# Kernel tuning notes

Measured on AMD Instinct MI355X. Metric: run time of the kernel, lower is better.

The kernel has to match this reference:

```python
import jax, jax.numpy as jnp
import numpy as np

U = 512  # units

def hard_sigmoid(x):
    # Keras hard_sigmoid: clip(0.2*x + 0.5, 0, 1)
    return jnp.clip(0.2 * x + 0.5, 0.0, 1.0)

def setup_inputs() -> dict:
    key = jax.random.key(0)
    ks = jax.random.split(key, 9)
    B, T, A, D = 64, 2048, 512, 512  # batch, annotation steps, annotation units, input dim
    s = lambda k, shape, scale: jax.random.normal(k, shape, jnp.float32) * scale
    return {
        "inputs": s(ks[0], (B, D), 1.0),
        "h": s(ks[1], (B, U), 1.0),
        "c": s(ks[2], (B, U), 1.0),
        "annotations": s(ks[3], (B, T, A), 1.0),
        "kernel": s(ks[4], (D + A, 4 * U), 0.02),
        "recurrent_kernel": s(ks[5], (U, 4 * U), 0.02),
        "bias": jnp.zeros((6 * U,), jnp.float32).at[U:2 * U].set(1.0),  # unit_forget_bias
        "kernel_u": s(ks[6], (A, U), 0.02),
        "kernel_w": s(ks[7], (U, U), 0.02),
        "kernel_v": s(ks[8], (U,), 0.02),
    }

def reference(inputs, h, c, annotations, kernel, recurrent_kernel, bias, kernel_u, kernel_w, kernel_v):
    bias_u = bias[4 * U:5 * U]
    # precomputed annotation projection (done once in build()): [B,T,U]
    uh = jnp.einsum('bta,au->btu', annotations, kernel_u) + bias_u
    # Bahdanau attention scores
    Wxstm = h @ kernel_w                                   # [B,U]
    et = jnp.einsum('btu,u->bt', jnp.tanh(uh + Wxstm[:, None, :]), kernel_v)
    at = jax.nn.softmax(et, axis=1)                        # exp/sum in source == softmax
    context = jnp.einsum('bt,bta->ba', at, annotations)    # [B,A]
    x = jnp.concatenate([inputs, context], axis=-1)        # [B, D+A]
    z = x @ kernel + h @ recurrent_kernel + bias[:4 * U]   # [B,4U]
    i = hard_sigmoid(z[:, :U])
    f = hard_sigmoid(z[:, U:2 * U])
    c_new = f * c + i * jnp.tanh(z[:, 2 * U:3 * U])
    o = hard_sigmoid(z[:, 3 * U:])
    h_new = o * jnp.tanh(c_new)
    return h_new
```

## Files before the change

### kernel.cpp

```cpp
#include <hip/hip_runtime.h>

constexpr int U = 512;
constexpr int B = 64;
constexpr int T = 2048;
constexpr int A = 512;

typedef __attribute__((ext_vector_type(8))) short short8;
typedef __attribute__((ext_vector_type(4))) float f32x4;

__device__ __forceinline__ unsigned short f32_to_bf16(float f) {
    unsigned int b = __float_as_uint(f);
    unsigned int r = (b + 0x7FFFu + ((b >> 16) & 1u)) >> 16;
    return (unsigned short)r;
}

__device__ __forceinline__ float fast_tanh(float x) {
    float e = exp2f(x * 2.885390081777927f);
    return (e - 1.0f) * __builtin_amdgcn_rcpf(e + 1.0f);
}

__device__ __forceinline__ float hard_sigmoid(float z) {
    return fminf(fmaxf(0.2f * z + 0.5f, 0.0f), 1.0f);
}

__global__ __launch_bounds__(256) void k_prep_s(const float* __restrict__ h,
                                                const float* __restrict__ kw,
                                                float* __restrict__ Sp) {
    int b = blockIdx.x >> 2;
    int kc = blockIdx.x & 3;
    int u = threadIdx.x;
    const float* hb = h + b * U + kc * 128;
    const float* kwb = kw + (size_t)kc * 128 * U;
    float a0 = 0.f, a1 = 0.f;
#pragma unroll 4
    for (int k = 0; k < 128; ++k) {
        float hv = hb[k];
        a0 += hv * kwb[(size_t)k * U + u];
        a1 += hv * kwb[(size_t)k * U + u + 256];
    }
    float* p = Sp + ((size_t)kc * 64 + b) * U;
    p[u] = a0;
    p[u + 256] = a1;
}

__global__ __launch_bounds__(256) void k_s_reduce(const float* __restrict__ Sp,
                                                  const float* __restrict__ bias,
                                                  float* __restrict__ S) {
    int gid = blockIdx.x * 256 + threadIdx.x;
    int b = gid >> 9, u = gid & 511;
    float s = bias[4 * U + u];
#pragma unroll
    for (int kc = 0; kc < 4; ++kc) s += Sp[((size_t)kc * 64 + b) * U + u];
    S[gid] = s;
}

__global__ __launch_bounds__(256) void k_prep_kut(const float* __restrict__ ku,
                                                  unsigned short* __restrict__ kut) {
    __shared__ float tile[32][33];
    int a0 = (blockIdx.x >> 4) << 5;
    int u0 = (blockIdx.x & 15) << 5;
    int c = threadIdx.x & 31, r0 = threadIdx.x >> 5;
#pragma unroll
    for (int p = 0; p < 4; ++p) {
        int r = r0 + p * 8;
        tile[r][c] = ku[(a0 + r) * U + u0 + c];
    }
    __syncthreads();
#pragma unroll
    for (int p = 0; p < 4; ++p) {
        int r = r0 + p * 8;
        kut[(u0 + r) * A + a0 + c] = f32_to_bf16(tile[c][r]);
    }
}

__global__ __launch_bounds__(256) void k_prep_wt(const float* __restrict__ kern,
                                                 const float* __restrict__ rk,
                                                 unsigned short* __restrict__ Wt) {
    __shared__ float tile[32][33];
    int k0 = blockIdx.x << 5;
    int j0 = blockIdx.y << 5;
    int c = threadIdx.x & 31, r0 = threadIdx.x >> 5;
#pragma unroll
    for (int p = 0; p < 4; ++p) {
        int r = r0 + p * 8;
        int k = k0 + r;
        float val = (k < 1024) ? kern[k * 2048 + j0 + c]
                               : rk[(k - 1024) * 2048 + j0 + c];
        tile[r][c] = val;
    }
    __syncthreads();
#pragma unroll
    for (int p = 0; p < 4; ++p) {
        int r = r0 + p * 8;
        Wt[(size_t)(j0 + r) * 1536 + k0 + c] = f32_to_bf16(tile[c][r]);
    }
}

__global__ __launch_bounds__(256, 2) void k_gemm_et(const float* __restrict__ ann,
                                                    const unsigned short* __restrict__ kut,
                                                    const float* __restrict__ S,
                                                    const float* __restrict__ v,
                                                    float* __restrict__ et) {
    __shared__ unsigned short As[64 * 64];
    __shared__ unsigned short Bs[512 * 64];
    __shared__ float red[4][64];

    const int tid = threadIdx.x;
    const int wave = tid >> 6;
    const int lane = tid & 63;
    const int lanelo = lane & 15;
    const int quad = lane >> 4;
    const int wn = wave;

    const int mt = blockIdx.x;
    const int b = mt >> 5;
    const int t0 = (mt & 31) << 6;
    const float* aBase = ann + (size_t)mt * 64 * A;

    f32x4 acc[4][8];
#pragma unroll
    for (int i = 0; i < 4; ++i)
#pragma unroll
        for (int j = 0; j < 8; ++j) acc[i][j] = {0.f, 0.f, 0.f, 0.f};

    f32x4 pv[4];
    const int rowA = tid >> 3;
    const int c8A = tid & 7;

#pragma unroll
    for (int q = 0; q < 2; ++q) {
        const float* src = aBase + (size_t)(q * 32 + rowA) * A + 0 + c8A * 8;
        pv[q * 2] = *(const f32x4*)src;
        pv[q * 2 + 1] = *(const f32x4*)(src + 4);
    }

    for (int k0 = 0; k0 < A; k0 += 64) {
#pragma unroll
        for (int p = 0; p < 16; ++p) {
            int seg = p * 4 + wave;
            int flat = seg * 1024 + lane * 16;
            int row = flat >> 7;
            int sc = (flat >> 4) & 7;
            int d = sc ^ (row & 7);
            __builtin_amdgcn_global_load_lds(
                (const __attribute__((address_space(1))) void*)(kut + (size_t)row * A + k0 + d * 8),
                (__attribute__((address_space(3))) void*)((char*)Bs + seg * 1024),
                16, 0, 0);
        }
#pragma unroll
        for (int q = 0; q < 2; ++q) {
            int row = q * 32 + rowA;
            f32x4 v0 = pv[q * 2], v1 = pv[q * 2 + 1];
            short8 pk;
            pk[0] = (short)f32_to_bf16(v0.x);
            pk[1] = (short)f32_to_bf16(v0.y);
            pk[2] = (short)f32_to_bf16(v0.z);
            pk[3] = (short)f32_to_bf16(v0.w);
            pk[4] = (short)f32_to_bf16(v1.x);
            pk[5] = (short)f32_to_bf16(v1.y);
            pk[6] = (short)f32_to_bf16(v1.z);
            pk[7] = (short)f32_to_bf16(v1.w);
            *(short8*)&As[row * 64 + ((c8A ^ (row & 7)) * 8)] = pk;
        }
        __syncthreads();
        if (k0 + 64 < A) {
#pragma unroll
            for (int q = 0; q < 2; ++q) {
                const float* src = aBase + (size_t)(q * 32 + rowA) * A + (k0 + 64) + c8A * 8;
                pv[q * 2] = *(const f32x4*)src;
                pv[q * 2 + 1] = *(const f32x4*)(src + 4);
            }
        }
#pragma unroll
        for (int s = 0; s < 2; ++s) {
            int c = s * 4 + quad;
            short8 af[4];
#pragma unroll
            for (int mi = 0; mi < 4; ++mi) {
                int row = mi * 16 + lanelo;
                af[mi] = *(const short8*)&As[row * 64 + ((c ^ (row & 7)) * 8)];
            }
            short8 bfr[8];
#pragma unroll
            for (int ni = 0; ni < 8; ++ni) {
                int rowb = wn * 128 + ni * 16 + lanelo;
                bfr[ni] = *(const short8*)&Bs[rowb * 64 + ((c ^ (rowb & 7)) * 8)];
            }
#pragma unroll
            for (int mi = 0; mi < 4; ++mi)
#pragma unroll
                for (int ni = 0; ni < 8; ++ni)
                    acc[mi][ni] = __builtin_amdgcn_mfma_f32_16x16x32_bf16(
                        af[mi], bfr[ni], acc[mi][ni], 0, 0, 0);
        }
        __syncthreads();
    }

    float rows[16];
#pragma unroll
    for (int i = 0; i < 16; ++i) rows[i] = 0.f;
#pragma unroll
    for (int ni = 0; ni < 8; ++ni) {
        int u = wn * 128 + ni * 16 + lanelo;
        float sv = S[b * U + u];
        float vv = v[u];
#pragma unroll
        for (int mi = 0; mi < 4; ++mi)
#pragma unroll
            for (int r = 0; r < 4; ++r)
                rows[mi * 4 + r] += fast_tanh(acc[mi][ni][r] + sv) * vv;
    }
#pragma unroll
    for (int i = 0; i < 16; ++i) {
        rows[i] += __shfl_xor(rows[i], 1);
        rows[i] += __shfl_xor(rows[i], 2);
        rows[i] += __shfl_xor(rows[i], 4);
        rows[i] += __shfl_xor(rows[i], 8);
    }
    if (lanelo == 0) {
#pragma unroll
        for (int mi = 0; mi < 4; ++mi)
#pragma unroll
            for (int r = 0; r < 4; ++r)
                red[wave][mi * 16 + quad * 4 + r] = rows[mi * 4 + r];
    }
    __syncthreads();
    if (tid < 64) {
        float sum = red[0][tid] + red[1][tid] + red[2][tid] + red[3][tid];
        et[b * T + t0 + tid] = sum;
    }
}

__global__ __launch_bounds__(256) void k_softmax(const float* __restrict__ et,
                                                 float* __restrict__ at) {
    __shared__ float sred[256];
    int b = blockIdx.x;
    const float* e = et + b * T;
    float vals[8];
    float mx = -1e30f;
#pragma unroll
    for (int i = 0; i < 8; ++i) {
        int t = threadIdx.x + i * 256;
        float x = e[t];
        vals[i] = x;
        mx = fmaxf(mx, x);
    }
    sred[threadIdx.x] = mx;
    __syncthreads();
    for (int s = 128; s > 0; s >>= 1) {
        if (threadIdx.x < s) sred[threadIdx.x] = fmaxf(sred[threadIdx.x], sred[threadIdx.x + s]);
        __syncthreads();
    }
    mx = sred[0];
    __syncthreads();
    float sum = 0.f;
#pragma unroll
    for (int i = 0; i < 8; ++i) {
        float x = exp2f((vals[i] - mx) * 1.4426950408889634f);
        vals[i] = x;
        sum += x;
    }
    sred[threadIdx.x] = sum;
    __syncthreads();
    for (int s = 128; s > 0; s >>= 1) {
        if (threadIdx.x < s) sred[threadIdx.x] += sred[threadIdx.x + s];
        __syncthreads();
    }
    float inv = 1.0f / sred[0];
#pragma unroll
    for (int i = 0; i < 8; ++i) at[b * T + threadIdx.x + i * 256] = vals[i] * inv;
}

__global__ __launch_bounds__(256) void k_ctx_part(const float* __restrict__ at,
                                                  const float* __restrict__ ann,
                                                  float* __restrict__ part) {
    __shared__ float buf[2][512];
    int b = blockIdx.x >> 3;
    int tc = blockIdx.x & 7;
    int half = threadIdx.x >> 7;
    int a4 = (threadIdx.x & 127) << 2;
    const float* annb = ann + ((size_t)b * T + tc * 256) * A;
    const float* atb = at + b * T + tc * 256;
    f32x4 acc = {0.f, 0.f, 0.f, 0.f};
    for (int t = half; t < 256; t += 2) {
        float w = atb[t];
        f32x4 rv = *(const f32x4*)(annb + (size_t)t * A + a4);
        acc.x += w * rv.x;
        acc.y += w * rv.y;
        acc.z += w * rv.z;
        acc.w += w * rv.w;
    }
    *(f32x4*)&buf[half][a4] = acc;
    __syncthreads();
    int a2 = threadIdx.x << 1;
    float s0 = buf[0][a2] + buf[1][a2];
    float s1 = buf[0][a2 + 1] + buf[1][a2 + 1];
    float* p = part + ((size_t)b * 8 + tc) * A;
    p[a2] = s0;
    p[a2 + 1] = s1;
}

__global__ __launch_bounds__(256) void k_ctx_reduce(const float* __restrict__ part,
                                                    float* __restrict__ ctx) {
    int b = blockIdx.x;
    for (int a = threadIdx.x; a < A; a += 256) {
        float s = 0.f;
#pragma unroll
        for (int c = 0; c < 8; ++c) s += part[((size_t)b * 8 + c) * A + a];
        ctx[b * A + a] = s;
    }
}

__global__ __launch_bounds__(256) void k_prep_xb(const float* __restrict__ inputs,
                                                 const float* __restrict__ ctx,
                                                 const float* __restrict__ h,
                                                 unsigned short* __restrict__ xb) {
    int b = blockIdx.y;
    int k = blockIdx.x * 256 + threadIdx.x;
    float val;
    if (k < 512) val = inputs[b * 512 + k];
    else if (k < 1024) val = ctx[b * 512 + (k - 512)];
    else val = h[b * 512 + (k - 1024)];
    xb[b * 1536 + k] = f32_to_bf16(val);
}

__global__ __launch_bounds__(256) void k_zgemm(const unsigned short* __restrict__ xb,
                                               const unsigned short* __restrict__ Wt,
                                               float* __restrict__ zpart) {
    const int kc = blockIdx.x & 7;
    const int nt = blockIdx.x >> 3;
    const int wave = threadIdx.x >> 6;
    const int lane = threadIdx.x & 63;
    const int lanelo = lane & 15;
    const int quad = lane >> 4;

    const int n = nt * 64 + wave * 16 + lanelo;
    const unsigned short* bp = Wt + (size_t)n * 1536 + kc * 192 + quad * 8;
    const unsigned short* ap = xb + (size_t)lanelo * 1536 + kc * 192 + quad * 8;

    f32x4 acc[4];
#pragma unroll
    for (int i = 0; i < 4; ++i) acc[i] = {0.f, 0.f, 0.f, 0.f};

#pragma unroll
    for (int ks = 0; ks < 6; ++ks) {
        short8 bfrag = *(const short8*)(bp + ks * 32);
#pragma unroll
        for (int mi = 0; mi < 4; ++mi) {
            short8 afrag = *(const short8*)(ap + (size_t)mi * 16 * 1536 + ks * 32);
            acc[mi] = __builtin_amdgcn_mfma_f32_16x16x32_bf16(afrag, bfrag, acc[mi], 0, 0, 0);
        }
    }

    float* p = zpart + (size_t)kc * 64 * 2048;
#pragma unroll
    for (int mi = 0; mi < 4; ++mi)
#pragma unroll
        for (int r = 0; r < 4; ++r) {
            int m = mi * 16 + quad * 4 + r;
            p[(size_t)m * 2048 + n] = acc[mi][r];
        }
}

__global__ __launch_bounds__(256) void k_gates(const float* __restrict__ zpart,
                                               const float* __restrict__ bias,
                                               const float* __restrict__ c,
                                               float* __restrict__ hnew) {
    int gid = blockIdx.x * 256 + threadIdx.x;
    int b = gid >> 9;
    int u = gid & 511;
    float z[4];
#pragma unroll
    for (int g = 0; g < 4; ++g) {
        int j = (g << 9) + u;
        float s = bias[j];
#pragma unroll
        for (int kc = 0; kc < 8; ++kc)
            s += zpart[((size_t)kc * 64 + b) * 2048 + j];
        z[g] = s;
    }
    float ig = hard_sigmoid(z[0]);
    float fg = hard_sigmoid(z[1]);
    float cn = fg * c[b * 512 + u] + ig * fast_tanh(z[2]);
    float og = hard_sigmoid(z[3]);
    hnew[b * 512 + u] = og * fast_tanh(cn);
}

extern "C" void kernel_launch(void* const* d_in, const int* in_sizes, int n_in,
                              void* d_out, int out_size, void* d_ws, size_t ws_size,
                              hipStream_t stream) {
    const float* inputs = (const float*)d_in[0];
    const float* h      = (const float*)d_in[1];
    const float* c      = (const float*)d_in[2];
    const float* ann    = (const float*)d_in[3];
    const float* kern   = (const float*)d_in[4];
    const float* rk     = (const float*)d_in[5];
    const float* bias   = (const float*)d_in[6];
    const float* ku     = (const float*)d_in[7];
    const float* kw     = (const float*)d_in[8];
    const float* kv     = (const float*)d_in[9];

    char* ws = (char*)d_ws;
    float*          S     = (float*)(ws + 0);
    unsigned short* kut   = (unsigned short*)(ws + 131072);
    float*          et    = (float*)(ws + 655360);
    float*          at    = (float*)(ws + 1703936);
    float*          part  = (float*)(ws + 2228224);
    float*          Sp    = (float*)(ws + 2228224);
    float*          ctx   = (float*)(ws + 3276800);
    unsigned short* xb    = (unsigned short*)(ws + 3407872);
    unsigned short* Wt    = (unsigned short*)(ws + 3604480);
    float*          zpart = (float*)(ws + 9895936);
    float*          hnew  = (float*)d_out;

    k_prep_wt<<<dim3(48, 64), 256, 0, stream>>>(kern, rk, Wt);
    k_prep_kut<<<256, 256, 0, stream>>>(ku, kut);
    k_prep_s<<<256, 256, 0, stream>>>(h, kw, Sp);
    k_s_reduce<<<128, 256, 0, stream>>>(Sp, bias, S);
    k_gemm_et<<<2048, 256, 0, stream>>>(ann, kut, S, kv, et);
    k_softmax<<<64, 256, 0, stream>>>(et, at);
    k_ctx_part<<<64 * 8, 256, 0, stream>>>(at, ann, part);
    k_ctx_reduce<<<64, 256, 0, stream>>>(part, ctx);
    k_prep_xb<<<dim3(6, 64), 256, 0, stream>>>(inputs, ctx, h, xb);
    k_zgemm<<<256, 256, 0, stream>>>(xb, Wt, zpart);
    k_gates<<<128, 256, 0, stream>>>(zpart, bias, c, hnew);
}
```

Before: 515.6 us.

## Double-buffer attention GEMM with K=32 stages and fuse small prep kernels

```diff
diff --git a/kernel.cpp b/kernel.cpp
--- a/kernel.cpp
+++ b/kernel.cpp
@@ -54,45 +54,45 @@
     S[gid] = s;
 }
 
-__global__ __launch_bounds__(256) void k_prep_kut(const float* __restrict__ ku,
-                                                  unsigned short* __restrict__ kut) {
+__global__ __launch_bounds__(256) void k_prep_wk(const float* __restrict__ kern,
+                                                 const float* __restrict__ rk,
+                                                 const float* __restrict__ ku,
+                                                 unsigned short* __restrict__ Wt,
+                                                 unsigned short* __restrict__ kut) {
     __shared__ float tile[32][33];
-    int a0 = (blockIdx.x >> 4) << 5;
-    int u0 = (blockIdx.x & 15) << 5;
+    int bid = blockIdx.x;
     int c = threadIdx.x & 31, r0 = threadIdx.x >> 5;
-#pragma unroll
-    for (int p = 0; p < 4; ++p) {
-        int r = r0 + p * 8;
-        tile[r][c] = ku[(a0 + r) * U + u0 + c];
-    }
-    __syncthreads();
-#pragma unroll
-    for (int p = 0; p < 4; ++p) {
-        int r = r0 + p * 8;
-        kut[(u0 + r) * A + a0 + c] = f32_to_bf16(tile[c][r]);
-    }
-}
-
-__global__ __launch_bounds__(256) void k_prep_wt(const float* __restrict__ kern,
-                                                 const float* __restrict__ rk,
-                                                 unsigned short* __restrict__ Wt) {
-    __shared__ float tile[32][33];
-    int k0 = blockIdx.x << 5;
-    int j0 = blockIdx.y << 5;
-    int c = threadIdx.x & 31, r0 = threadIdx.x >> 5;
-#pragma unroll
-    for (int p = 0; p < 4; ++p) {
-        int r = r0 + p * 8;
-        int k = k0 + r;
-        float val = (k < 1024) ? kern[k * 2048 + j0 + c]
-                               : rk[(k - 1024) * 2048 + j0 + c];
-        tile[r][c] = val;
-    }
-    __syncthreads();
-#pragma unroll
-    for (int p = 0; p < 4; ++p) {
-        int r = r0 + p * 8;
-        Wt[(size_t)(j0 + r) * 1536 + k0 + c] = f32_to_bf16(tile[c][r]);
+    if (bid < 3072) {
+        int kt = bid % 48, jt = bid / 48;
+        int k0 = kt << 5, j0 = jt << 5;
+#pragma unroll
+        for (int p = 0; p < 4; ++p) {
+            int r = r0 + p * 8;
+            int k = k0 + r;
+            float val = (k < 1024) ? kern[k * 2048 + j0 + c]
+                                   : rk[(k - 1024) * 2048 + j0 + c];
+            tile[r][c] = val;
+        }
+        __syncthreads();
+#pragma unroll
+        for (int p = 0; p < 4; ++p) {
+            int r = r0 + p * 8;
+            Wt[(size_t)(j0 + r) * 1536 + k0 + c] = f32_to_bf16(tile[c][r]);
+        }
+    } else {
+        int q = bid - 3072;
+        int a0 = (q >> 4) << 5, u0 = (q & 15) << 5;
+#pragma unroll
+        for (int p = 0; p < 4; ++p) {
+            int r = r0 + p * 8;
+            tile[r][c] = ku[(a0 + r) * U + u0 + c];
+        }
+        __syncthreads();
+#pragma unroll
+        for (int p = 0; p < 4; ++p) {
+            int r = r0 + p * 8;
+            kut[(u0 + r) * A + a0 + c] = f32_to_bf16(tile[c][r]);
+        }
     }
 }
 
@@ -101,8 +101,8 @@
                                                     const float* __restrict__ S,
                                                     const float* __restrict__ v,
                                                     float* __restrict__ et) {
-    __shared__ unsigned short As[64 * 64];
-    __shared__ unsigned short Bs[512 * 64];
+    __shared__ unsigned short Bs[2][512 * 32];
+    __shared__ unsigned short As[2][64 * 32];
     __shared__ float red[4][64];
 
     const int tid = threadIdx.x;
@@ -117,82 +117,96 @@
     const int t0 = (mt & 31) << 6;
     const float* aBase = ann + (size_t)mt * 64 * A;
 
+    const int rowA = tid >> 2;
+    const int c8A = tid & 3;
+    const int slotA = c8A ^ (rowA & 3) ^ ((rowA >> 2) & 3);
+    const float* aSrc = aBase + (size_t)rowA * A + c8A * 8;
+
     f32x4 acc[4][8];
 #pragma unroll
     for (int i = 0; i < 4; ++i)
 #pragma unroll
         for (int j = 0; j < 8; ++j) acc[i][j] = {0.f, 0.f, 0.f, 0.f};
 
-    f32x4 pv[4];
-    const int rowA = tid >> 3;
-    const int c8A = tid & 7;
-
-#pragma unroll
-    for (int q = 0; q < 2; ++q) {
-        const float* src = aBase + (size_t)(q * 32 + rowA) * A + 0 + c8A * 8;
-        pv[q * 2] = *(const f32x4*)src;
-        pv[q * 2 + 1] = *(const f32x4*)(src + 4);
-    }
-
-    for (int k0 = 0; k0 < A; k0 += 64) {
-#pragma unroll
-        for (int p = 0; p < 16; ++p) {
+    {
+#pragma unroll
+        for (int p = 0; p < 8; ++p) {
             int seg = p * 4 + wave;
             int flat = seg * 1024 + lane * 16;
-            int row = flat >> 7;
-            int sc = (flat >> 4) & 7;
-            int d = sc ^ (row & 7);
+            int row = flat >> 6;
+            int sc = (flat >> 4) & 3;
+            int d = sc ^ (row & 3) ^ ((row >> 2) & 3);
             __builtin_amdgcn_global_load_lds(
-                (const __attribute__((address_space(1))) void*)(kut + (size_t)row * A + k0 + d * 8),
-                (__attribute__((address_space(3))) void*)((char*)Bs + seg * 1024),
+                (const __attribute__((address_space(1))) void*)(kut + (size_t)row * A + 0 + d * 8),
+                (__attribute__((address_space(3))) void*)((char*)&Bs[0][0] + seg * 1024),
                 16, 0, 0);
         }
-#pragma unroll
-        for (int q = 0; q < 2; ++q) {
-            int row = q * 32 + rowA;
-            f32x4 v0 = pv[q * 2], v1 = pv[q * 2 + 1];
+        f32x4 a0 = *(const f32x4*)(aSrc);
+        f32x4 a1 = *(const f32x4*)(aSrc + 4);
+        short8 pk;
+        pk[0] = (short)f32_to_bf16(a0.x); pk[1] = (short)f32_to_bf16(a0.y);
+        pk[2] = (short)f32_to_bf16(a0.z); pk[3] = (short)f32_to_bf16(a0.w);
+        pk[4] = (short)f32_to_bf16(a1.x); pk[5] = (short)f32_to_bf16(a1.y);
+        pk[6] = (short)f32_to_bf16(a1.z); pk[7] = (short)f32_to_bf16(a1.w);
+        *(short8*)&As[0][rowA * 32 + slotA * 8] = pk;
+    }
+    f32x4 pvb0 = *(const f32x4*)(aSrc + 32);
+    f32x4 pvb1 = *(const f32x4*)(aSrc + 36);
+    __syncthreads();
+
+#pragma unroll
+    for (int it = 0; it < 16; ++it) {
+        const int cur = it & 1;
+        const int nxt = cur ^ 1;
+        if (it + 1 < 16) {
+#pragma unroll
+            for (int p = 0; p < 8; ++p) {
+                int seg = p * 4 + wave;
+                int flat = seg * 1024 + lane * 16;
+                int row = flat >> 6;
+                int sc = (flat >> 4) & 3;
+                int d = sc ^ (row & 3) ^ ((row >> 2) & 3);
+                __builtin_amdgcn_global_load_lds(
+                    (const __attribute__((address_space(1))) void*)(kut + (size_t)row * A + (it + 1) * 32 + d * 8),
+                    (__attribute__((address_space(3))) void*)((char*)&Bs[nxt][0] + seg * 1024),
+                    16, 0, 0);
+            }
+        }
+        f32x4 nv0 = {0.f, 0.f, 0.f, 0.f}, nv1 = {0.f, 0.f, 0.f, 0.f};
+        if (it + 2 < 16) {
+            nv0 = *(const f32x4*)(aSrc + (it + 2) * 32);
+            nv1 = *(const f32x4*)(aSrc + (it + 2) * 32 + 4);
+        }
+        short8 af[4];
+#pragma unroll
+        for (int mi = 0; mi < 4; ++mi) {
+            int row = mi * 16 + lanelo;
+            int slot = quad ^ (row & 3) ^ ((row >> 2) & 3);
+            af[mi] = *(const short8*)&As[cur][row * 32 + slot * 8];
+        }
+        short8 bfr[8];
+#pragma unroll
+        for (int ni = 0; ni < 8; ++ni) {
+            int rowb = wn * 128 + ni * 16 + lanelo;
+            int slot = quad ^ (rowb & 3) ^ ((rowb >> 2) & 3);
+            bfr[ni] = *(const short8*)&Bs[cur][rowb * 32 + slot * 8];
+        }
+#pragma unroll
+        for (int mi = 0; mi < 4; ++mi)
+#pragma unroll
+            for (int ni = 0; ni < 8; ++ni)
+                acc[mi][ni] = __builtin_amdgcn_mfma_f32_16x16x32_bf16(
+                    af[mi], bfr[ni], acc[mi][ni], 0, 0, 0);
+        if (it + 1 < 16) {
             short8 pk;
-            pk[0] = (short)f32_to_bf16(v0.x);
-            pk[1] = (short)f32_to_bf16(v0.y);
-            pk[2] = (short)f32_to_bf16(v0.z);
-            pk[3] = (short)f32_to_bf16(v0.w);
-            pk[4] = (short)f32_to_bf16(v1.x);
-            pk[5] = (short)f32_to_bf16(v1.y);
-            pk[6] = (short)f32_to_bf16(v1.z);
-            pk[7] = (short)f32_to_bf16(v1.w);
-            *(short8*)&As[row * 64 + ((c8A ^ (row & 7)) * 8)] = pk;
-        }
-        __syncthreads();
-        if (k0 + 64 < A) {
-#pragma unroll
-            for (int q = 0; q < 2; ++q) {
-                const float* src = aBase + (size_t)(q * 32 + rowA) * A + (k0 + 64) + c8A * 8;
-                pv[q * 2] = *(const f32x4*)src;
-                pv[q * 2 + 1] = *(const f32x4*)(src + 4);
-            }
-        }
-#pragma unroll
-        for (int s = 0; s < 2; ++s) {
-            int c = s * 4 + quad;
-            short8 af[4];
-#pragma unroll
-            for (int mi = 0; mi < 4; ++mi) {
-                int row = mi * 16 + lanelo;
-                af[mi] = *(const short8*)&As[row * 64 + ((c ^ (row & 7)) * 8)];
-            }
-            short8 bfr[8];
-#pragma unroll
-            for (int ni = 0; ni < 8; ++ni) {
-                int rowb = wn * 128 + ni * 16 + lanelo;
-                bfr[ni] = *(const short8*)&Bs[rowb * 64 + ((c ^ (rowb & 7)) * 8)];
-            }
-#pragma unroll
-            for (int mi = 0; mi < 4; ++mi)
-#pragma unroll
-                for (int ni = 0; ni < 8; ++ni)
-                    acc[mi][ni] = __builtin_amdgcn_mfma_f32_16x16x32_bf16(
-                        af[mi], bfr[ni], acc[mi][ni], 0, 0, 0);
-        }
+            pk[0] = (short)f32_to_bf16(pvb0.x); pk[1] = (short)f32_to_bf16(pvb0.y);
+            pk[2] = (short)f32_to_bf16(pvb0.z); pk[3] = (short)f32_to_bf16(pvb0.w);
+            pk[4] = (short)f32_to_bf16(pvb1.x); pk[5] = (short)f32_to_bf16(pvb1.y);
+            pk[6] = (short)f32_to_bf16(pvb1.z); pk[7] = (short)f32_to_bf16(pvb1.w);
+            *(short8*)&As[nxt][rowA * 32 + slotA * 8] = pk;
+        }
+        pvb0 = nv0;
+        pvb1 = nv1;
         __syncthreads();
     }
 
@@ -300,28 +314,19 @@
     p[a2 + 1] = s1;
 }
 
-__global__ __launch_bounds__(256) void k_ctx_reduce(const float* __restrict__ part,
-                                                    float* __restrict__ ctx) {
+__global__ __launch_bounds__(512) void k_ctx_xb(const float* __restrict__ part,
+                                                const float* __restrict__ inputs,
+                                                const float* __restrict__ h,
+                                                unsigned short* __restrict__ xb) {
     int b = blockIdx.x;
-    for (int a = threadIdx.x; a < A; a += 256) {
-        float s = 0.f;
-#pragma unroll
-        for (int c = 0; c < 8; ++c) s += part[((size_t)b * 8 + c) * A + a];
-        ctx[b * A + a] = s;
-    }
-}
-
-__global__ __launch_bounds__(256) void k_prep_xb(const float* __restrict__ inputs,
-                                                 const float* __restrict__ ctx,
-                                                 const float* __restrict__ h,
-                                                 unsigned short* __restrict__ xb) {
-    int b = blockIdx.y;
-    int k = blockIdx.x * 256 + threadIdx.x;
-    float val;
-    if (k < 512) val = inputs[b * 512 + k];
-    else if (k < 1024) val = ctx[b * 512 + (k - 512)];
-    else val = h[b * 512 + (k - 1024)];
-    xb[b * 1536 + k] = f32_to_bf16(val);
+    int u = threadIdx.x;
+    float s = 0.f;
+#pragma unroll
+    for (int c = 0; c < 8; ++c) s += part[((size_t)b * 8 + c) * A + u];
+    unsigned short* x = xb + (size_t)b * 1536;
+    x[u] = f32_to_bf16(inputs[b * 512 + u]);
+    x[512 + u] = f32_to_bf16(s);
+    x[1024 + u] = f32_to_bf16(h[b * 512 + u]);
 }
 
 __global__ __launch_bounds__(256) void k_zgemm(const unsigned short* __restrict__ xb,
@@ -407,21 +412,18 @@
     float*          at    = (float*)(ws + 1703936);
     float*          part  = (float*)(ws + 2228224);
     float*          Sp    = (float*)(ws + 2228224);
-    float*          ctx   = (float*)(ws + 3276800);
     unsigned short* xb    = (unsigned short*)(ws + 3407872);
     unsigned short* Wt    = (unsigned short*)(ws + 3604480);
     float*          zpart = (float*)(ws + 9895936);
     float*          hnew  = (float*)d_out;
 
-    k_prep_wt<<<dim3(48, 64), 256, 0, stream>>>(kern, rk, Wt);
-    k_prep_kut<<<256, 256, 0, stream>>>(ku, kut);
+    k_prep_wk<<<3328, 256, 0, stream>>>(kern, rk, ku, Wt, kut);
     k_prep_s<<<256, 256, 0, stream>>>(h, kw, Sp);
     k_s_reduce<<<128, 256, 0, stream>>>(Sp, bias, S);
     k_gemm_et<<<2048, 256, 0, stream>>>(ann, kut, S, kv, et);
     k_softmax<<<64, 256, 0, stream>>>(et, at);
     k_ctx_part<<<64 * 8, 256, 0, stream>>>(at, ann, part);
-    k_ctx_reduce<<<64, 256, 0, stream>>>(part, ctx);
-    k_prep_xb<<<dim3(6, 64), 256, 0, stream>>>(inputs, ctx, h, xb);
+    k_ctx_xb<<<64, 512, 0, stream>>>(part, inputs, h, xb);
     k_zgemm<<<256, 256, 0, stream>>>(xb, Wt, zpart);
     k_gates<<<128, 256, 0, stream>>>(zpart, bias, c, hnew);
 }
```

New measurement: 597.1 us. +15.8%, slower.
